# Optimization experiments

Measured on AMD Instinct MI355X. Metric: run time of the kernel, lower is better.

Reference implementation:

```python
import jax, jax.numpy as jnp
import numpy as np
import math

B, LQ, LK, D = 8, 4096, 32768, 64
LKS = min(8000, LK)                                    # sampled key window (K[:, :8000])
UPART = min(5 * LQ * int(np.ceil(np.log1p(LKS))), LKS)  # = 8000


def setup_inputs() -> dict:
    key = jax.random.key(0)
    k1, k2, k3, k4 = jax.random.split(key, 4)
    q = jax.random.normal(k1, (B, LQ, D), dtype=jnp.float32)
    K = jax.random.normal(k2, (B, LK, D), dtype=jnp.float32)
    V = jax.random.normal(k3, (B, LK, D), dtype=jnp.float32)
    index_sample = jax.random.randint(k4, (UPART,), 0, LKS)  # torch.randint(0, L_K, (U_part,))
    return {"q": q, "K": K, "V": V, "index_sample": index_sample}


def reference(q, K, V, index_sample):
    L_K = min(8000, K.shape[1])            # K_sample = K[:, :8000]; L_K = K_sample.size(1)
    L_Q = q.shape[1]
    d_k = q.shape[-1]
    log_L_Q = int(np.ceil(np.log1p(L_Q)))
    u = min(5 * log_L_Q, L_Q)

    # gather sampled keys (indices < 8000, indexing full K as in the source)
    K_samp = K[:, index_sample, :]                         # [B, U_part, D]
    QKs = jnp.einsum('bqd,bud->bqu', q, K_samp)            # [B, L_Q, U_part]
    # sparsity measure: max - mean (divided by L_K as in torch.div(sum, L_K))
    M = QKs.max(axis=-1) - QKs.sum(axis=-1) / L_K          # [B, L_Q]
    # torch topk(largest=False) -> smallest u values of M
    _, M_top = jax.lax.top_k(-M, u)                        # [B, u]
    Q_reduce = jnp.take_along_axis(q, M_top[:, :, None], axis=1)  # [B, u, D]

    attn_scores = jnp.einsum('bud,bkd->buk', Q_reduce, K) / math.sqrt(d_k)  # [B, u, L_K_full]
    attn_probs = jax.nn.softmax(attn_scores, axis=-1)
    attn_output = jnp.einsum('buk,bkd->bud', attn_probs, V)                  # [B, u, D]
    return attn_output, attn_scores
```

## Files before the change

kernel.cpp:

```cpp
#include <hip/hip_runtime.h>

#define BB 8
#define LQ 4096
#define LK 32768
#define DD 64
#define UU 8000
#define NU 45
#define TQ2 128
#define TUC 160
#define NCH (UU/TUC)
#define CHB (TUC*DD*2)
#define KT5 512
#define NT5 64

typedef short short8 __attribute__((ext_vector_type(8)));
typedef float floatx16 __attribute__((ext_vector_type(16)));

__device__ __forceinline__ float bf2f(unsigned short h){ return __uint_as_float(((unsigned int)h) << 16); }
__device__ __forceinline__ unsigned short f2bf(float f){
  unsigned int u = __float_as_uint(f);
  u += 0x7FFFu + ((u >> 16) & 1u);
  return (unsigned short)(u >> 16);
}
__device__ __forceinline__ unsigned int fkey(float v){
  unsigned int u = __float_as_uint(v);
  return (u & 0x80000000u) ? ~u : (u | 0x80000000u);
}

__global__ __launch_bounds__(256) void k_gather(const float* __restrict__ Kg, const int* __restrict__ idx,
                                                unsigned short* __restrict__ khi, unsigned short* __restrict__ kmid){
  const int b = blockIdx.y;
  const int row = blockIdx.x*32 + (threadIdx.x >> 3);
  const int oct = threadIdx.x & 7;
  const float* src = Kg + ((size_t)(b*LK + idx[row]))*DD + oct*8;
  float x[8];
  #pragma unroll
  for (int j=0;j<8;j++) x[j] = src[j];
  unsigned short h[8], m[8];
  #pragma unroll
  for (int j=0;j<8;j++){
    h[j] = f2bf(x[j]);
    m[j] = f2bf(x[j] - bf2f(h[j]));
  }
  const int osl = oct ^ (row & 7);
  size_t o = ((size_t)(b*UU + row))*DD + osl*8;
  #pragma unroll
  for (int j=0;j<8;j++){ khi[o+j]=h[j]; kmid[o+j]=m[j]; }
}

__global__ __launch_bounds__(64) void k_spart(const float* __restrict__ Kg, const int* __restrict__ idx,
                                              float* __restrict__ Spart){
  const int g = blockIdx.x, b = blockIdx.y, d = threadIdx.x;
  float acc = 0.0f;
  for (int j=0;j<64;j++){
    int u = g*64 + j;
    acc += Kg[((size_t)(b*LK + idx[u]))*DD + d];
  }
  Spart[((size_t)(b*125 + g))*DD + d] = acc;
}
__global__ __launch_bounds__(64) void k_sred(const float* __restrict__ Spart, float* __restrict__ Sb){
  const int b = blockIdx.x, d = threadIdx.x;
  float acc = 0.0f;
  for (int g=0; g<125; g++) acc += Spart[((size_t)(b*125 + g))*DD + d];
  Sb[b*DD + d] = acc;
}

__device__ __forceinline__ void stage_chunk(const char* gh, const char* gm,
                                            unsigned short* Bhb, unsigned short* Bmb,
                                            int w, int lane){
  #pragma unroll
  for (int i=0;i<5;i++){
    const int u = w*5 + i;
    if (u < 20){
      __builtin_amdgcn_global_load_lds(
        (const __attribute__((address_space(1))) void*)(gh + u*1024 + lane*16),
        (__attribute__((address_space(3))) void*)((char*)Bhb + u*1024 + lane*16),
        16, 0, 0);
    } else {
      __builtin_amdgcn_global_load_lds(
        (const __attribute__((address_space(1))) void*)(gm + (u-20)*1024 + lane*16),
        (__attribute__((address_space(3))) void*)((char*)Bmb + (u-20)*1024 + lane*16),
        16, 0, 0);
    }
  }
}

__global__ __launch_bounds__(512,2) void k_Mm(const float* __restrict__ q,
                                              const unsigned short* __restrict__ khi,
                                              const unsigned short* __restrict__ kmid,
                                              float* __restrict__ amaxG, int* __restrict__ acargG){
  const int qt = blockIdx.x, b = blockIdx.y;
  const int tid = threadIdx.x;
  const int w = tid >> 6, lane = tid & 63;
  const int tr = w & 3, sp = w >> 2;
  const int l31 = lane & 31, lh = lane >> 5;
  __shared__ __align__(16) unsigned short Bh[2][TUC*DD];
  __shared__ __align__(16) unsigned short Bm[2][TUC*DD];
  __shared__ float combV[TQ2][2];
  __shared__ int   combC[TQ2][2];

  const int qrow = qt*TQ2 + tr*32 + l31;
  short8 ahi[4], amid[4];
  {
    const float* qp = q + ((size_t)(b*LQ) + qrow)*DD;
    #pragma unroll
    for (int s=0;s<4;s++){
      const int d0 = s*16 + lh*8;
      float4 x0 = *(const float4*)(qp + d0);
      float4 x1 = *(const float4*)(qp + d0 + 4);
      float xs[8] = {x0.x,x0.y,x0.z,x0.w,x1.x,x1.y,x1.z,x1.w};
      short8 h, m;
      #pragma unroll
      for (int j=0;j<8;j++){
        unsigned short hb = f2bf(xs[j]);
        unsigned short mb = f2bf(xs[j] - bf2f(hb));
        h[j] = (short)hb; m[j] = (short)mb;
      }
      ahi[s]=h; amid[s]=m;
    }
  }

  float vmax[16]; int carg[16];
  #pragma unroll
  for (int r=0;r<16;r++){ vmax[r]=-INFINITY; carg[r]=0; }

  const size_t kbyte = (size_t)b*UU*DD*2;
  const char* ghbase = (const char*)khi + kbyte;
  const char* gmbase = (const char*)kmid + kbyte;

  stage_chunk(ghbase, gmbase, &Bh[0][0], &Bm[0][0], w, lane);
  int cur = 0;

  for (int c=0;c<NCH;c++){
    __syncthreads();
    if (c+1 < NCH){
      stage_chunk(ghbase + (size_t)(c+1)*CHB, gmbase + (size_t)(c+1)*CHB,
                  &Bh[cur^1][0], &Bm[cur^1][0], w, lane);
    }
    float lmax[16];
    #pragma unroll
    for (int r=0;r<16;r++) lmax[r] = -INFINITY;
    for (int t = ((c ^ sp) & 1); t < 5; t += 2){
      floatx16 accA = {0.f,0.f,0.f,0.f,0.f,0.f,0.f,0.f,0.f,0.f,0.f,0.f,0.f,0.f,0.f,0.f};
      floatx16 accB = {0.f,0.f,0.f,0.f,0.f,0.f,0.f,0.f,0.f,0.f,0.f,0.f,0.f,0.f,0.f,0.f};
      #pragma unroll
      for (int s=0;s<4;s++){
        const int eo = (t*32 + l31)*DD + (((s*2 + lh) ^ (l31 & 7))*8);
        short8 bh = *(const short8*)(&Bh[cur][eo]);
        short8 bm = *(const short8*)(&Bm[cur][eo]);
        if (s & 1){
          accB = __builtin_amdgcn_mfma_f32_32x32x16_bf16(amid[s], bh, accB, 0, 0, 0);
          accB = __builtin_amdgcn_mfma_f32_32x32x16_bf16(ahi[s],  bm, accB, 0, 0, 0);
          accB = __builtin_amdgcn_mfma_f32_32x32x16_bf16(ahi[s],  bh, accB, 0, 0, 0);
        } else {
          accA = __builtin_amdgcn_mfma_f32_32x32x16_bf16(amid[s], bh, accA, 0, 0, 0);
          accA = __builtin_amdgcn_mfma_f32_32x32x16_bf16(ahi[s],  bm, accA, 0, 0, 0);
          accA = __builtin_amdgcn_mfma_f32_32x32x16_bf16(ahi[s],  bh, accA, 0, 0, 0);
        }
      }
      #pragma unroll
      for (int r=0;r<16;r++) lmax[r] = fmaxf(lmax[r], accA[r] + accB[r]);
    }
    #pragma unroll
    for (int r=0;r<16;r++){
      if (lmax[r] > vmax[r]){ vmax[r] = lmax[r]; carg[r] = c; }
    }
    cur ^= 1;
  }
  #pragma unroll
  for (int st=1; st<32; st<<=1){
    #pragma unroll
    for (int r=0;r<16;r++){
      float ov = __shfl_xor(vmax[r], st);
      int   oc = __shfl_xor(carg[r], st);
      if (ov > vmax[r]){ vmax[r]=ov; carg[r]=oc; }
    }
  }
  if (l31 == 0){
    #pragma unroll
    for (int r=0;r<16;r++){
      int m = (r&3) + 8*(r>>2) + 4*lh;
      int ql = tr*32 + m;
      combV[ql][sp] = vmax[r];
      combC[ql][sp] = carg[r];
    }
  }
  __syncthreads();
  if (tid < TQ2){
    float v0 = combV[tid][0], v1 = combV[tid][1];
    int   c0 = combC[tid][0], c1 = combC[tid][1];
    bool t1 = v1 > v0;
    amaxG[(size_t)b*LQ + qt*TQ2 + tid] = t1 ? v1 : v0;
    acargG[(size_t)b*LQ + qt*TQ2 + tid] = t1 ? c1 : c0;
  }
}

__global__ __launch_bounds__(256,4) void k_ref(const float* __restrict__ q, const float* __restrict__ Kg,
                                               const int* __restrict__ idx, const float* __restrict__ Sb,
                                               const int* __restrict__ acargG, float* __restrict__ M){
  const int w = threadIdx.x >> 6, lane = threadIdx.x & 63;
  const int gq = blockIdx.x*4 + w;
  const int b = gq >> 12;
  const int quad = lane & 3;
  const int rg = lane >> 2;

  const float* qp = q + (size_t)gq*DD + quad*16;
  float4 q0 = ((const float4*)qp)[0];
  float4 q1 = ((const float4*)qp)[1];
  float4 q2 = ((const float4*)qp)[2];
  float4 q3 = ((const float4*)qp)[3];

  const int base = acargG[gq]*TUC;
  const int* ip = idx + base + rg;
  int rows[10];
  #pragma unroll
  for (int p=0;p<10;p++) rows[p] = ip[p*16];

  const float* kbase = Kg + (size_t)b*LK*DD + quad*16;
  float mx = -INFINITY;
  #pragma unroll
  for (int p=0;p<10;p++){
    const float* kp = kbase + (size_t)rows[p]*DD;
    float4 k0 = ((const float4*)kp)[0];
    float4 k1 = ((const float4*)kp)[1];
    float4 k2 = ((const float4*)kp)[2];
    float4 k3 = ((const float4*)kp)[3];
    float a0 = q0.x*k0.x, a1 = q0.y*k0.y, a2 = q0.z*k0.z, a3 = q0.w*k0.w;
    a0 = fmaf(q1.x,k1.x,a0); a1 = fmaf(q1.y,k1.y,a1); a2 = fmaf(q1.z,k1.z,a2); a3 = fmaf(q1.w,k1.w,a3);
    a0 = fmaf(q2.x,k2.x,a0); a1 = fmaf(q2.y,k2.y,a1); a2 = fmaf(q2.z,k2.z,a2); a3 = fmaf(q2.w,k2.w,a3);
    a0 = fmaf(q3.x,k3.x,a0); a1 = fmaf(q3.y,k3.y,a1); a2 = fmaf(q3.z,k3.z,a2); a3 = fmaf(q3.w,k3.w,a3);
    float s = (a0+a1)+(a2+a3);
    s += __shfl_xor(s, 1);
    s += __shfl_xor(s, 2);
    mx = fmaxf(mx, s);
  }
  #pragma unroll
  for (int st=4; st<64; st<<=1) mx = fmaxf(mx, __shfl_xor(mx, st));

  const float* sp = Sb + b*DD + quad*16;
  float4 s0 = ((const float4*)sp)[0];
  float4 s1 = ((const float4*)sp)[1];
  float4 s2 = ((const float4*)sp)[2];
  float4 s3 = ((const float4*)sp)[3];
  float m0 = q0.x*s0.x, m1 = q0.y*s0.y, m2 = q0.z*s0.z, m3 = q0.w*s0.w;
  m0 = fmaf(q1.x,s1.x,m0); m1 = fmaf(q1.y,s1.y,m1); m2 = fmaf(q1.z,s1.z,m2); m3 = fmaf(q1.w,s1.w,m3);
  m0 = fmaf(q2.x,s2.x,m0); m1 = fmaf(q2.y,s2.y,m1); m2 = fmaf(q2.z,s2.z,m2); m3 = fmaf(q2.w,s2.w,m3);
  m0 = fmaf(q3.x,s3.x,m0); m1 = fmaf(q3.y,s3.y,m1); m2 = fmaf(q3.z,s3.z,m2); m3 = fmaf(q3.w,s3.w,m3);
  float ms = (m0+m1)+(m2+m3);
  ms += __shfl_xor(ms, 1);
  ms += __shfl_xor(ms, 2);
  if (lane == 0){
    M[gq] = mx - ms * (1.0f/8000.0f);
  }
}

__global__ __launch_bounds__(256) void k_select(const float* __restrict__ Mg,
                                                const float* __restrict__ q,
                                                int* __restrict__ MtopG, float* __restrict__ Qred){
  const int b = blockIdx.x, tid = threadIdx.x;
  __shared__ float Mv[LQ];
  __shared__ unsigned long long wmin[4];
  __shared__ int mtop[NU];
  __shared__ int selB;
  for (int qq = tid; qq < LQ; qq += 256) Mv[qq] = Mg[(size_t)b*LQ + qq];
  __syncthreads();
  unsigned long long lm = ~0ull;
  #pragma unroll
  for (int i=0;i<16;i++){
    int qq = tid + 256*i;
    unsigned long long kk = (((unsigned long long)fkey(Mv[qq]))<<32) | (unsigned int)qq;
    lm = (kk < lm) ? kk : lm;
  }
  for (int i=0;i<NU;i++){
    unsigned long long v = lm;
    #pragma unroll
    for (int st=1; st<64; st<<=1){
      unsigned long long o = __shfl_xor(v, st);
      v = (o < v) ? o : v;
    }
    if ((tid & 63) == 0) wmin[tid>>6] = v;
    __syncthreads();
    if (tid == 0){
      unsigned long long g01 = (wmin[0] < wmin[1]) ? wmin[0] : wmin[1];
      unsigned long long g23 = (wmin[2] < wmin[3]) ? wmin[2] : wmin[3];
      unsigned long long g = (g01 < g23) ? g01 : g23;
      int sel = (int)(g & 0xFFFFFFFFull);
      mtop[i] = sel; selB = sel; Mv[sel] = INFINITY;
    }
    __syncthreads();
    int sel = selB;
    if (tid == (sel & 255)){
      unsigned long long nl = ~0ull;
      #pragma unroll
      for (int j=0;j<16;j++){
        int qq = tid + 256*j;
        unsigned long long kk = (((unsigned long long)fkey(Mv[qq]))<<32) | (unsigned int)qq;
        nl = (kk < nl) ? kk : nl;
      }
      lm = nl;
    }
    __syncthreads();
  }
  if (tid < NU) MtopG[b*NU + tid] = mtop[tid];
  for (int e = tid; e < NU*DD; e += 256){
    int ui = e >> 6, d = e & 63;
    Qred[((size_t)(b*NU + ui))*DD + d] = q[((size_t)(b*LQ + mtop[ui]))*DD + d];
  }
}

#define QFMA(i) { float4 p = qr4[i]; \
  a0 = fmaf(kv##i.x, p.x, a0); a1 = fmaf(kv##i.y, p.y, a1); \
  a2 = fmaf(kv##i.z, p.z, a2); a3 = fmaf(kv##i.w, p.w, a3); }

__global__ __launch_bounds__(256) void k_scores(const float* __restrict__ Kg,
                                                const float* __restrict__ Qred,
                                                float* __restrict__ out1){
  const int b = blockIdx.y;
  const int k = blockIdx.x*256 + threadIdx.x;
  const float4* kp4 = (const float4*)(Kg + ((size_t)(b*LK + k))*DD);
  const float4 kv0  = kp4[0],  kv1  = kp4[1],  kv2  = kp4[2],  kv3  = kp4[3];
  const float4 kv4  = kp4[4],  kv5  = kp4[5],  kv6  = kp4[6],  kv7  = kp4[7];
  const float4 kv8  = kp4[8],  kv9  = kp4[9],  kv10 = kp4[10], kv11 = kp4[11];
  const float4 kv12 = kp4[12], kv13 = kp4[13], kv14 = kp4[14], kv15 = kp4[15];
  for (int u=0; u<NU; u++){
    const float4* qr4 = (const float4*)(Qred + ((size_t)(b*NU+u))*DD);
    float a0 = 0.f, a1 = 0.f, a2 = 0.f, a3 = 0.f;
    QFMA(0)  QFMA(1)  QFMA(2)  QFMA(3)
    QFMA(4)  QFMA(5)  QFMA(6)  QFMA(7)
    QFMA(8)  QFMA(9)  QFMA(10) QFMA(11)
    QFMA(12) QFMA(13) QFMA(14) QFMA(15)
    float s = ((a0+a1)+(a2+a3)) * 0.125f;
    out1[((size_t)(b*NU+u)<<15) + k] = s;
  }
}

__global__ __launch_bounds__(256) void k_rowstats(const float* __restrict__ out1,
                                                  float* __restrict__ rowm, float* __restrict__ rowinvl){
  const int r = blockIdx.x, tid = threadIdx.x;
  const float* row = out1 + ((size_t)r << 15);
  __shared__ float red[256];
  float mx = -INFINITY;
  for (int k = tid; k < LK; k += 256) mx = fmaxf(mx, row[k]);
  red[tid] = mx; __syncthreads();
  for (int s=128;s>0;s>>=1){ if (tid<s) red[tid] = fmaxf(red[tid], red[tid+s]); __syncthreads(); }
  float m = red[0]; __syncthreads();
  float sm = 0.0f;
  for (int k = tid; k < LK; k += 256) sm += __expf(row[k] - m);
  red[tid] = sm; __syncthreads();
  for (int s=128;s>0;s>>=1){ if (tid<s) red[tid] += red[tid+s]; __syncthreads(); }
  if (tid==0){ rowm[r] = m; rowinvl[r] = 1.0f/red[0]; }
}

__global__ __launch_bounds__(512) void k_pv(const float* __restrict__ Vg,
                                            const float* __restrict__ out1,
                                            const float* __restrict__ rowm, const float* __restrict__ rowinvl,
                                            float* __restrict__ pvpart){
  const int kt = blockIdx.x, b = blockIdx.y, tid = threadIdx.x;
  const int lane = tid & 63, w = tid >> 6;
  const int u0 = w*6;
  __shared__ float Vl[128][65];
  __shared__ __align__(16) float Pl[48][132];
  float acc[6];
  #pragma unroll
  for (int j=0;j<6;j++) acc[j] = 0.0f;
  for (int sc=0; sc<4; sc++){
    const int k0 = kt*KT5 + sc*128;
    {
      int r = tid >> 2, h = tid & 3;
      const float* vp = Vg + ((size_t)(b*LK + k0 + r))*DD + h*16;
      #pragma unroll
      for (int j=0;j<4;j++){
        float4 t = ((const float4*)vp)[j];
        Vl[r][h*16 + 4*j]   = t.x;
        Vl[r][h*16 + 4*j+1] = t.y;
        Vl[r][h*16 + 4*j+2] = t.z;
        Vl[r][h*16 + 4*j+3] = t.w;
      }
    }
    for (int e = tid; e < 48*128; e += 512){
      int u = e >> 7, kk = e & 127;
      float p = 0.0f;
      if (u < NU){
        int r = b*NU + u;
        float s = out1[((size_t)r<<15) + k0 + kk];
        p = __expf(s - rowm[r]) * rowinvl[r];
      }
      Pl[u][kk] = p;
    }
    __syncthreads();
    for (int kk4=0; kk4<32; kk4++){
      float v0 = Vl[4*kk4+0][lane];
      float v1 = Vl[4*kk4+1][lane];
      float v2 = Vl[4*kk4+2][lane];
      float v3 = Vl[4*kk4+3][lane];
      #pragma unroll
      for (int j=0;j<6;j++){
        float4 p = *reinterpret_cast<const float4*>(&Pl[u0+j][4*kk4]);
        acc[j] = fmaf(p.w, v3, fmaf(p.z, v2, fmaf(p.y, v1, fmaf(p.x, v0, acc[j]))));
      }
    }
    __syncthreads();
  }
  #pragma unroll
  for (int j=0;j<6;j++){
    if (u0 + j < NU){
      pvpart[(((size_t)(b*NU + u0 + j))*NT5 + kt)*DD + lane] = acc[j];
    }
  }
}

__global__ __launch_bounds__(256) void k_final(const float* __restrict__ pvpart, float* __restrict__ out0){
  int e = blockIdx.x*256 + threadIdx.x;
  if (e >= BB*NU*DD) return;
  int d = e & 63; int r = e >> 6;
  float s = 0.0f;
  for (int t=0;t<NT5;t++) s += pvpart[((size_t)r*NT5 + t)*DD + d];
  out0[e] = s;
}

extern "C" void kernel_launch(void* const* d_in, const int* in_sizes, int n_in,
                              void* d_out, int out_size, void* d_ws, size_t ws_size,
                              hipStream_t stream){
  const float* q  = (const float*)d_in[0];
  const float* K  = (const float*)d_in[1];
  const float* V  = (const float*)d_in[2];
  const int* idx  = (const int*)d_in[3];
  float* out0 = (float*)d_out;
  float* out1 = out0 + BB*NU*DD;

  float* ws = (float*)d_ws;
  unsigned short* khi  = (unsigned short*)ws;
  float*  pvpart = ws;
  unsigned short* kmid = (unsigned short*)(ws + (size_t)BB*UU*DD/2);
  float* Spart   = ws + (size_t)BB*UU*DD;
  float* Sb      = Spart + 64000;
  float* amax    = Sb + 512;
  int*   acarg   = (int*)(amax + BB*LQ);
  float* Mbq     = (float*)(acarg + BB*LQ);
  float* Qred    = Mbq + BB*LQ;
  float* rowm    = Qred + (size_t)BB*NU*DD;
  float* rowinvl = rowm + 512;
  int*   Mtop    = (int*)(rowinvl + 512);

  k_gather<<<dim3(UU/32, BB), 256, 0, stream>>>(K, idx, khi, kmid);
  k_spart<<<dim3(125, BB), 64, 0, stream>>>(K, idx, Spart);
  k_sred<<<BB, 64, 0, stream>>>(Spart, Sb);
  k_Mm<<<dim3(LQ/TQ2, BB), 512, 0, stream>>>(q, khi, kmid, amax, acarg);
  k_ref<<<BB*LQ/4, 256, 0, stream>>>(q, K, idx, Sb, acarg, Mbq);
  k_select<<<BB, 256, 0, stream>>>(Mbq, q, Mtop, Qred);
  k_scores<<<dim3(LK/256, BB), 256, 0, stream>>>(K, Qred, out1);
  k_rowstats<<<BB*NU, 256, 0, stream>>>(out1, rowm, rowinvl);
  k_pv<<<dim3(NT5, BB), 512, 0, stream>>>(V, out1, rowm, rowinvl, pvpart);
  k_final<<<(BB*NU*DD + 255)/256, 256, 0, stream>>>(pvpart, out0);
}
```

Baseline: 607.0 us.

## Bucket queries by argmax chunk and refine from LDS-staged key chunks

A new bucketing kernel groups each batch's queries by the key chunk that holds their approximate max, using a shared-memory histogram and scatter. The refinement kernel then runs one block per (chunk, batch). Each block loads that chunk's 160 gathered key rows into XOR-swizzled LDS once and evaluates every query in the bucket, two queries per wave. Before, every query re-gathered its own 10 rows from global memory. The change adds an extra launch and atomics, and blocks can be unevenly loaded if bucket sizes vary.

```diff
diff --git a/kernel.cpp b/kernel.cpp
--- a/kernel.cpp
+++ b/kernel.cpp
@@ -195,62 +195,117 @@
   }
 }
 
-__global__ __launch_bounds__(256,4) void k_ref(const float* __restrict__ q, const float* __restrict__ Kg,
-                                               const int* __restrict__ idx, const float* __restrict__ Sb,
-                                               const int* __restrict__ acargG, float* __restrict__ M){
-  const int w = threadIdx.x >> 6, lane = threadIdx.x & 63;
-  const int gq = blockIdx.x*4 + w;
-  const int b = gq >> 12;
-  const int quad = lane & 3;
-  const int rg = lane >> 2;
-
-  const float* qp = q + (size_t)gq*DD + quad*16;
-  float4 q0 = ((const float4*)qp)[0];
-  float4 q1 = ((const float4*)qp)[1];
-  float4 q2 = ((const float4*)qp)[2];
-  float4 q3 = ((const float4*)qp)[3];
-
-  const int base = acargG[gq]*TUC;
-  const int* ip = idx + base + rg;
-  int rows[10];
-  #pragma unroll
-  for (int p=0;p<10;p++) rows[p] = ip[p*16];
-
-  const float* kbase = Kg + (size_t)b*LK*DD + quad*16;
-  float mx = -INFINITY;
-  #pragma unroll
-  for (int p=0;p<10;p++){
-    const float* kp = kbase + (size_t)rows[p]*DD;
-    float4 k0 = ((const float4*)kp)[0];
-    float4 k1 = ((const float4*)kp)[1];
-    float4 k2 = ((const float4*)kp)[2];
-    float4 k3 = ((const float4*)kp)[3];
-    float a0 = q0.x*k0.x, a1 = q0.y*k0.y, a2 = q0.z*k0.z, a3 = q0.w*k0.w;
-    a0 = fmaf(q1.x,k1.x,a0); a1 = fmaf(q1.y,k1.y,a1); a2 = fmaf(q1.z,k1.z,a2); a3 = fmaf(q1.w,k1.w,a3);
-    a0 = fmaf(q2.x,k2.x,a0); a1 = fmaf(q2.y,k2.y,a1); a2 = fmaf(q2.z,k2.z,a2); a3 = fmaf(q2.w,k2.w,a3);
-    a0 = fmaf(q3.x,k3.x,a0); a1 = fmaf(q3.y,k3.y,a1); a2 = fmaf(q3.z,k3.z,a2); a3 = fmaf(q3.w,k3.w,a3);
-    float s = (a0+a1)+(a2+a3);
-    s += __shfl_xor(s, 1);
-    s += __shfl_xor(s, 2);
-    mx = fmaxf(mx, s);
-  }
-  #pragma unroll
-  for (int st=4; st<64; st<<=1) mx = fmaxf(mx, __shfl_xor(mx, st));
-
-  const float* sp = Sb + b*DD + quad*16;
-  float4 s0 = ((const float4*)sp)[0];
-  float4 s1 = ((const float4*)sp)[1];
-  float4 s2 = ((const float4*)sp)[2];
-  float4 s3 = ((const float4*)sp)[3];
-  float m0 = q0.x*s0.x, m1 = q0.y*s0.y, m2 = q0.z*s0.z, m3 = q0.w*s0.w;
-  m0 = fmaf(q1.x,s1.x,m0); m1 = fmaf(q1.y,s1.y,m1); m2 = fmaf(q1.z,s1.z,m2); m3 = fmaf(q1.w,s1.w,m3);
-  m0 = fmaf(q2.x,s2.x,m0); m1 = fmaf(q2.y,s2.y,m1); m2 = fmaf(q2.z,s2.z,m2); m3 = fmaf(q2.w,s2.w,m3);
-  m0 = fmaf(q3.x,s3.x,m0); m1 = fmaf(q3.y,s3.y,m1); m2 = fmaf(q3.z,s3.z,m2); m3 = fmaf(q3.w,s3.w,m3);
-  float ms = (m0+m1)+(m2+m3);
-  ms += __shfl_xor(ms, 1);
-  ms += __shfl_xor(ms, 2);
-  if (lane == 0){
-    M[gq] = mx - ms * (1.0f/8000.0f);
+__global__ __launch_bounds__(256) void k_bucket(const int* __restrict__ acargG,
+                                                int* __restrict__ qlist, int* __restrict__ bstart){
+  const int b = blockIdx.x, tid = threadIdx.x;
+  __shared__ int cnt[NCH];
+  __shared__ int pos[NCH];
+  if (tid < NCH) cnt[tid] = 0;
+  __syncthreads();
+  for (int qq = tid; qq < LQ; qq += 256){
+    int ch = acargG[(size_t)b*LQ + qq];
+    ch = (ch < 0) ? 0 : ((ch >= NCH) ? NCH-1 : ch);
+    atomicAdd(&cnt[ch], 1);
+  }
+  __syncthreads();
+  if (tid == 0){
+    int acc = 0;
+    for (int c=0;c<NCH;c++){ pos[c] = acc; bstart[b*64 + c] = acc; acc += cnt[c]; }
+    bstart[b*64 + NCH] = acc;
+  }
+  __syncthreads();
+  for (int qq = tid; qq < LQ; qq += 256){
+    int ch = acargG[(size_t)b*LQ + qq];
+    ch = (ch < 0) ? 0 : ((ch >= NCH) ? NCH-1 : ch);
+    int p = atomicAdd(&pos[ch], 1);
+    p = (p < 0) ? 0 : ((p >= LQ) ? LQ-1 : p);
+    qlist[(size_t)b*LQ + p] = qq;
+  }
+}
+
+__global__ __launch_bounds__(256,3) void k_refb(const float* __restrict__ q, const float* __restrict__ Kg,
+                                                const int* __restrict__ idx, const float* __restrict__ Sb,
+                                                const int* __restrict__ qlist, const int* __restrict__ bstart,
+                                                float* __restrict__ M){
+  const int ch = blockIdx.x, b = blockIdx.y;
+  const int tid = threadIdx.x;
+  const int w = tid >> 6, lane = tid & 63;
+  const int quad = lane & 3, rg = lane >> 2;
+  __shared__ __align__(16) float Kl[TUC*DD];
+  float4* Kl4 = (float4*)Kl;
+  for (int g = tid; g < TUC*16; g += 256){
+    int row = g >> 4, s = g & 15;
+    int gidx = idx[ch*TUC + row];
+    float4 v = *(const float4*)(Kg + ((size_t)(b*LK + gidx))*DD + s*4);
+    Kl4[row*16 + (s ^ (row & 7))] = v;
+  }
+  __syncthreads();
+
+  const float4* sp4 = (const float4*)(Sb + b*DD + quad*16);
+  const float4 S0 = sp4[0], S1 = sp4[1], S2 = sp4[2], S3 = sp4[3];
+  const int sl0 = ((quad<<2)|0) ^ (rg & 7);
+  const int sl1 = ((quad<<2)|1) ^ (rg & 7);
+  const int sl2 = ((quad<<2)|2) ^ (rg & 7);
+  const int sl3 = ((quad<<2)|3) ^ (rg & 7);
+  const int rbs = rg*16;
+  const int s0 = bstart[b*64 + ch], s1 = bstart[b*64 + ch + 1];
+
+  for (int i = s0 + (w<<1); i < s1; i += 8){
+    const int qa = qlist[(size_t)b*LQ + i];
+    const int i2 = (i+1 < s1) ? i+1 : i;
+    const int qb = qlist[(size_t)b*LQ + i2];
+    const float4* ap = (const float4*)(q + ((size_t)(b*LQ + qa))*DD + quad*16);
+    const float4* bp = (const float4*)(q + ((size_t)(b*LQ + qb))*DD + quad*16);
+    const float4 A0 = ap[0], A1 = ap[1], A2 = ap[2], A3 = ap[3];
+    const float4 B0 = bp[0], B1 = bp[1], B2 = bp[2], B3 = bp[3];
+    float mxa = -INFINITY, mxb = -INFINITY;
+    #pragma unroll
+    for (int p=0;p<10;p++){
+      const int base = p*256 + rbs;
+      float4 k0 = Kl4[base + sl0];
+      float4 k1 = Kl4[base + sl1];
+      float4 k2 = Kl4[base + sl2];
+      float4 k3 = Kl4[base + sl3];
+      float a0 = A0.x*k0.x, a1 = A0.y*k0.y, a2 = A0.z*k0.z, a3 = A0.w*k0.w;
+      a0 = fmaf(A1.x,k1.x,a0); a1 = fmaf(A1.y,k1.y,a1); a2 = fmaf(A1.z,k1.z,a2); a3 = fmaf(A1.w,k1.w,a3);
+      a0 = fmaf(A2.x,k2.x,a0); a1 = fmaf(A2.y,k2.y,a1); a2 = fmaf(A2.z,k2.z,a2); a3 = fmaf(A2.w,k2.w,a3);
+      a0 = fmaf(A3.x,k3.x,a0); a1 = fmaf(A3.y,k3.y,a1); a2 = fmaf(A3.z,k3.z,a2); a3 = fmaf(A3.w,k3.w,a3);
+      float c0 = B0.x*k0.x, c1 = B0.y*k0.y, c2 = B0.z*k0.z, c3 = B0.w*k0.w;
+      c0 = fmaf(B1.x,k1.x,c0); c1 = fmaf(B1.y,k1.y,c1); c2 = fmaf(B1.z,k1.z,c2); c3 = fmaf(B1.w,k1.w,c3);
+      c0 = fmaf(B2.x,k2.x,c0); c1 = fmaf(B2.y,k2.y,c1); c2 = fmaf(B2.z,k2.z,c2); c3 = fmaf(B2.w,k2.w,c3);
+      c0 = fmaf(B3.x,k3.x,c0); c1 = fmaf(B3.y,k3.y,c1); c2 = fmaf(B3.z,k3.z,c2); c3 = fmaf(B3.w,k3.w,c3);
+      float sa = (a0+a1)+(a2+a3);
+      float sc = (c0+c1)+(c2+c3);
+      sa += __shfl_xor(sa, 1);
+      sa += __shfl_xor(sa, 2);
+      sc += __shfl_xor(sc, 1);
+      sc += __shfl_xor(sc, 2);
+      mxa = fmaxf(mxa, sa);
+      mxb = fmaxf(mxb, sc);
+    }
+    #pragma unroll
+    for (int st=4; st<64; st<<=1){
+      mxa = fmaxf(mxa, __shfl_xor(mxa, st));
+      mxb = fmaxf(mxb, __shfl_xor(mxb, st));
+    }
+    float m0 = A0.x*S0.x, m1 = A0.y*S0.y, m2 = A0.z*S0.z, m3 = A0.w*S0.w;
+    m0 = fmaf(A1.x,S1.x,m0); m1 = fmaf(A1.y,S1.y,m1); m2 = fmaf(A1.z,S1.z,m2); m3 = fmaf(A1.w,S1.w,m3);
+    m0 = fmaf(A2.x,S2.x,m0); m1 = fmaf(A2.y,S2.y,m1); m2 = fmaf(A2.z,S2.z,m2); m3 = fmaf(A2.w,S2.w,m3);
+    m0 = fmaf(A3.x,S3.x,m0); m1 = fmaf(A3.y,S3.y,m1); m2 = fmaf(A3.z,S3.z,m2); m3 = fmaf(A3.w,S3.w,m3);
+    float msa = (m0+m1)+(m2+m3);
+    msa += __shfl_xor(msa, 1);
+    msa += __shfl_xor(msa, 2);
+    float n0 = B0.x*S0.x, n1 = B0.y*S0.y, n2 = B0.z*S0.z, n3 = B0.w*S0.w;
+    n0 = fmaf(B1.x,S1.x,n0); n1 = fmaf(B1.y,S1.y,n1); n2 = fmaf(B1.z,S1.z,n2); n3 = fmaf(B1.w,S1.w,n3);
+    n0 = fmaf(B2.x,S2.x,n0); n1 = fmaf(B2.y,S2.y,n1); n2 = fmaf(B2.z,S2.z,n2); n3 = fmaf(B2.w,S2.w,n3);
+    n0 = fmaf(B3.x,S3.x,n0); n1 = fmaf(B3.y,S3.y,n1); n2 = fmaf(B3.z,S3.z,n2); n3 = fmaf(B3.w,S3.w,n3);
+    float msb = (n0+n1)+(n2+n3);
+    msb += __shfl_xor(msb, 1);
+    msb += __shfl_xor(msb, 2);
+    if (lane == 0){
+      M[(size_t)b*LQ + qa] = mxa - msa * (1.0f/8000.0f);
+      if (i2 != i) M[(size_t)b*LQ + qb] = mxb - msb * (1.0f/8000.0f);
+    }
   }
 }
 
@@ -441,12 +496,15 @@
   float* rowm    = Qred + (size_t)BB*NU*DD;
   float* rowinvl = rowm + 512;
   int*   Mtop    = (int*)(rowinvl + 512);
+  int*   qlist   = Mtop + 512;
+  int*   bstart  = qlist + (size_t)BB*LQ;
 
   k_gather<<<dim3(UU/32, BB), 256, 0, stream>>>(K, idx, khi, kmid);
   k_spart<<<dim3(125, BB), 64, 0, stream>>>(K, idx, Spart);
   k_sred<<<BB, 64, 0, stream>>>(Spart, Sb);
   k_Mm<<<dim3(LQ/TQ2, BB), 512, 0, stream>>>(q, khi, kmid, amax, acarg);
-  k_ref<<<BB*LQ/4, 256, 0, stream>>>(q, K, idx, Sb, acarg, Mbq);
+  k_bucket<<<BB, 256, 0, stream>>>(acarg, qlist, bstart);
+  k_refb<<<dim3(NCH, BB), 256, 0, stream>>>(q, K, idx, Sb, qlist, bstart, Mbq);
   k_select<<<BB, 256, 0, stream>>>(Mbq, q, Mtop, Qred);
   k_scores<<<dim3(LK/256, BB), 256, 0, stream>>>(K, Qred, out1);
   k_rowstats<<<BB*NU, 256, 0, stream>>>(out1, rowm, rowinvl);
```

Measured after the change: 616.6 us. No clear change (+1.6%).
